# Optimization experiments

Measured on AMD Instinct MI355X. Metric: run time of the kernel, lower is better.

The kernel has to match this reference:

```python
import jax, jax.numpy as jnp
import numpy as np

GS_ITERS = 10
GS_TAU = 0.5
NEG = -1e9
B, L, D, H = 4, 512, 64, 128


def gphi_scores(x, W1, b1, W2, b2):
    # Faithful to: concat([x_i, x_j]) -> Linear(2D,H) -> ReLU -> Linear(H,1).squeeze(-1)
    # Linear on the concat of [x_i, x_j] == x_i @ W1[:D] + x_j @ W1[D:] (fused, no [B,L,L,2D] tensor).
    d = x.shape[-1]
    pi = jnp.einsum('bld,dh->blh', x, W1[:d])   # row-index half of concat
    pj = jnp.einsum('bld,dh->blh', x, W1[d:])   # col-index half of concat
    h = jax.nn.relu(pi[:, :, None, :] + pj[:, None, :, :] + b1)  # [B,L,L,H]
    return jnp.einsum('blmh,h->blm', h, W2[:, 0]) + b2[0]        # [B,L,L]


def gumbel_sinkhorn(log_alpha, gumbel, pad_mask, tau, n_iters):
    # (scores + gumbel noise)/tau, mask padded rows/cols, alternate row/col log-normalization.
    la = (log_alpha + gumbel) / tau
    la = jnp.where(pad_mask, NEG, la)

    def step(la, _):
        la = la - jax.nn.logsumexp(la, axis=2, keepdims=True)  # row normalize
        la = la - jax.nn.logsumexp(la, axis=1, keepdims=True)  # col normalize
        la = jnp.where(pad_mask, NEG, la)
        return la, None

    la, _ = jax.lax.scan(step, la, None, length=n_iters)
    return jnp.exp(la)


def make_pad_mask(seq_lens, max_len):
    # mask_map logic: for a sequence of length s, rows < s have cols < s valid; rows >= s fully invalid.
    ar = jnp.arange(max_len)
    s = seq_lens[:, None, None]
    valid = (ar[None, :, None] < s) & (ar[None, None, :] < s)
    return ~valid  # True where gumbel-masked


def setup_inputs() -> dict:
    key = jax.random.key(0)
    ks = jax.random.split(key, 8)
    event_time = jax.random.uniform(ks[0], (B, L), dtype=jnp.float32) * 10.0
    event_type = jax.random.randint(ks[1], (B, L), 0, 50, dtype=jnp.int32)
    clean_enc_out = jax.random.normal(ks[2], (B, L, D), dtype=jnp.float32)
    seq_lens = jax.random.randint(ks[3], (B,), 1, L + 1, dtype=jnp.int32)
    u = jax.random.uniform(ks[4], (B, L, L), dtype=jnp.float32, minval=1e-6, maxval=1.0 - 1e-6)
    gumbel_noise = -jnp.log(-jnp.log(u))
    # gphi_mlp params (xavier-ish scaling)
    W1 = jax.random.normal(ks[5], (2 * D, H), dtype=jnp.float32) * (1.0 / np.sqrt(2 * D))
    b1 = jnp.full((H,), 0.01, dtype=jnp.float32)
    W2 = jax.random.normal(ks[6], (H, 1), dtype=jnp.float32) * (1.0 / np.sqrt(H))
    b2 = jnp.full((1,), 0.01, dtype=jnp.float32)
    return {"event_time": event_time, "event_type": event_type,
            "clean_enc_out": clean_enc_out, "seq_lens": seq_lens,
            "gumbel_noise": gumbel_noise, "W1": W1, "b1": b1, "W2": W2, "b2": b2}


def reference(event_time, event_type, clean_enc_out, seq_lens, gumbel_noise, W1, b1, W2, b2):
    pad_mask = make_pad_mask(seq_lens, event_time.shape[1])
    scores = gphi_scores(clean_enc_out, W1, b1, W2, b2)           # [B,L,L]
    perm = gumbel_sinkhorn(scores, gumbel_noise, pad_mask, GS_TAU, GS_ITERS)
    # same_perm_matrix=True, no_time_noise=True path
    types_permed = jnp.einsum('bl,blm->bm', event_type.astype(jnp.float32), perm)
    times_permed = jnp.einsum('bl,blm->bm', event_time, perm)
    return types_permed, times_permed, perm
```

## Files before the change

kernel.cpp:

```cpp
#include <hip/hip_runtime.h>
#include <cstdint>

#define BB 4
#define LL 512
#define DD 64
#define HH 128
#define NEGV -1000000000.0f
#define NBLK 256
#define NTHR 1024
#define NACT 64

union U8 { unsigned long long u; float2 f; };

__device__ __forceinline__ float2 cload_f2(const float* p) {
    U8 v;
    v.u = __hip_atomic_load((const unsigned long long*)p,
                            __ATOMIC_RELAXED, __HIP_MEMORY_SCOPE_AGENT);
    return v.f;
}
__device__ __forceinline__ void cstore_f2(float* p, float2 x) {
    U8 v; v.f = x;
    __hip_atomic_store((unsigned long long*)p, v.u,
                       __ATOMIC_RELAXED, __HIP_MEMORY_SCOPE_AGENT);
}

__device__ __forceinline__ void grid_barrier(unsigned* cnt, unsigned target) {
    __builtin_amdgcn_fence(__ATOMIC_RELEASE, "workgroup");
    __syncthreads();
    if (threadIdx.x == 0) {
        __hip_atomic_fetch_add(cnt, 1u, __ATOMIC_RELAXED, __HIP_MEMORY_SCOPE_AGENT);
        while (__hip_atomic_load(cnt, __ATOMIC_RELAXED, __HIP_MEMORY_SCOPE_AGENT) < target)
            __builtin_amdgcn_s_sleep(1);
    }
    __builtin_amdgcn_fence(__ATOMIC_ACQUIRE, "workgroup");
    __syncthreads();
}

__device__ __forceinline__ float hmax4(float4 v) {
    return fmaxf(fmaxf(v.x, v.y), fmaxf(v.z, v.w));
}

__global__ __launch_bounds__(NTHR) void mega(
    const float* __restrict__ etime, const int* __restrict__ etype,
    const float* __restrict__ x, const int* __restrict__ slens,
    const float* __restrict__ gum, const float* __restrict__ W1,
    const float* __restrict__ b1, const float* __restrict__ W2,
    const float* __restrict__ b2, float* __restrict__ out, float* __restrict__ ws)
{
    __shared__ float smem[19072];

    unsigned* cntA = (unsigned*)ws;
    float* piG   = ws + 128;
    float* pjG   = piG + BB * LL * HH;
    float* laG   = pjG + BB * LL * HH;
    float* cpkG  = laG + (size_t)BB * LL * LL;
    float* poutG = cpkG + (size_t)2 * BB * 16 * LL * 2;

    const int t = threadIdx.x;
    const int bx = blockIdx.x;

    {
        int gid = (bx << 10) + t;
        int arr = gid >> 17;
        int rem = gid & 131071;
        int row = rem >> 6;
        int h0  = (rem & 63) << 1;
        const float* xr = x + row * DD;
        const float* wb = W1 + (size_t)(arr * DD) * HH + h0;
        float a0 = arr ? 0.f : b1[h0];
        float a1 = arr ? 0.f : b1[h0 + 1];
        #pragma unroll 8
        for (int d = 0; d < DD; ++d) {
            float xv = xr[d];
            a0 = fmaf(xv, wb[d * HH + 0], a0);
            a1 = fmaf(xv, wb[d * HH + 1], a1);
        }
        float* dst = (arr ? pjG : piG) + (size_t)row * HH + h0;
        cstore_f2(dst, make_float2(a0, a1));
    }
    grid_barrier(cntA, 1 * NBLK);

    {
        float* sp  = smem;
        float* sq  = smem + 8192;
        float* sw2 = smem + 18944;
        int jt = bx & 7, it8 = (bx >> 3) & 7, b = bx >> 6;
        int i0 = it8 << 6, j0 = jt << 6;
        int rowb = b * LL + i0, colb = b * LL + j0;

        #pragma unroll
        for (int k = 0; k < 8; ++k) {
            int idx = (k << 10) + t;
            int buf = idx >> 12;
            int u   = idx & 4095;
            int row = u >> 6;
            int du  = u & 63;
            int q   = du >> 1;
            int hi  = du & 1;
            int dq  = q ^ ((row >> 2) & 7);
            const float* src = (buf ? pjG + (size_t)(colb + row) * HH
                                    : piG + (size_t)(rowb + row) * HH) + (du << 1);
            float2 v = cload_f2(src);
            float* dst = (buf ? sq : sp) + row * HH + (dq << 2) + (hi << 1);
            *(float2*)dst = v;
        }
        if (t < HH) sw2[t] = W2[t];
        __syncthreads();

        int hg = t >> 8, tt = t & 255;
        int w = tt >> 6, lane = tt & 63;
        int ti = ((w >> 1) << 3) + (lane >> 3);
        int tj = ((w & 1) << 3) + (lane & 7);
        int kti = ti & 7, ktj = tj & 7;

        float acc[4][4];
        #pragma unroll
        for (int a = 0; a < 4; ++a)
            #pragma unroll
            for (int c = 0; c < 4; ++c) acc[a][c] = 0.f;

        for (int hq = hg * 8; hq < hg * 8 + 8; ++hq) {
            float4 w4 = *(const float4*)(sw2 + (hq << 2));
            int offi = (hq ^ kti) << 2;
            int offj = (hq ^ ktj) << 2;
            float4 pa[4], pb[4];
            #pragma unroll
            for (int a = 0; a < 4; ++a) pa[a] = *(const float4*)(sp + (4*ti + a) * HH + offi);
            #pragma unroll
            for (int c = 0; c < 4; ++c) pb[c] = *(const float4*)(sq + (4*tj + c) * HH + offj);
            #pragma unroll
            for (int a = 0; a < 4; ++a) {
                #pragma unroll
                for (int c = 0; c < 4; ++c) {
                    float t0 = fmaxf(pa[a].x + pb[c].x, 0.f);
                    float t1 = fmaxf(pa[a].y + pb[c].y, 0.f);
                    float t2 = fmaxf(pa[a].z + pb[c].z, 0.f);
                    float t3 = fmaxf(pa[a].w + pb[c].w, 0.f);
                    float s = acc[a][c];
                    s += t0 * w4.x; s += t1 * w4.y; s += t2 * w4.z; s += t3 * w4.w;
                    acc[a][c] = s;
                }
            }
        }
        __syncthreads();
        float* cbuf = smem;
        #pragma unroll
        for (int a = 0; a < 4; ++a)
            #pragma unroll
            for (int c = 0; c < 4; ++c)
                cbuf[(((hg << 8) + tt) << 4) + (a << 2) + c] = acc[a][c];
        __syncthreads();

        int tt2 = t >> 2, a2 = t & 3;
        int w2_ = tt2 >> 6, lane2 = tt2 & 63;
        int ti2 = ((w2_ >> 1) << 3) + (lane2 >> 3);
        int tj2 = ((w2_ & 1) << 3) + (lane2 & 7);
        float4 o = make_float4(0.f, 0.f, 0.f, 0.f);
        #pragma unroll
        for (int g = 0; g < 4; ++g) {
            float4 pp = *(const float4*)(cbuf + (((g << 8) + tt2) << 4) + (a2 << 2));
            o.x += pp.x; o.y += pp.y; o.z += pp.z; o.w += pp.w;
        }
        int sl = slens[b];
        float bb2 = b2[0];
        int ig = i0 + 4 * ti2 + a2;
        int jb = j0 + 4 * tj2;
        float4 g4 = *(const float4*)(gum + ((size_t)(b * LL + ig)) * LL + jb);
        bool iv = ig < sl;
        float4 res;
        res.x = (iv && (jb + 0) < sl) ? (o.x + bb2 + g4.x) * 2.0f : NEGV;
        res.y = (iv && (jb + 1) < sl) ? (o.y + bb2 + g4.y) * 2.0f : NEGV;
        res.z = (iv && (jb + 2) < sl) ? (o.z + bb2 + g4.z) * 2.0f : NEGV;
        res.w = (iv && (jb + 3) < sl) ? (o.w + bb2 + g4.w) * 2.0f : NEGV;
        float* lap = laG + ((size_t)(b * LL + ig)) * LL + jb;
        cstore_f2(lap,     make_float2(res.x, res.y));
        cstore_f2(lap + 2, make_float2(res.z, res.w));
    }
    grid_barrier(cntA, 2 * NBLK);

    if (bx >= NACT) return;

    const int b2i = bx >> 4;
    const int stripe = bx & 15;
    const int r0 = stripe << 5;
    unsigned* cntB = (unsigned*)ws + 16 + (b2i << 4);
    float* sla  = smem;
    float* redm = smem + 16384;
    float* reds = smem + 17408;
    float* clse = smem + 18432;
    const int sl_a = slens[b2i];
    float tyv = 0.f, tmv = 0.f;

    {
        const float* src = laG + (((size_t)(b2i << 9) + r0) << 9);
        #pragma unroll
        for (int k = 0; k < 8; ++k) {
            int u = (k << 10) + t;
            float2 v = cload_f2(src + (u << 1));
            *(float2*)(sla + (u << 1)) = v;
        }
        __syncthreads();
    }

    for (int it = 0; it < 10; ++it) {
        const int par = it & 1;
        const int last = (it == 9);
        {
            int r = t >> 5, cq = t & 31;
            float4 v[4];
            #pragma unroll
            for (int k = 0; k < 4; ++k)
                v[k] = *(float4*)(sla + (r << 9) + ((cq + (k << 5)) << 2));
            float m = fmaxf(fmaxf(hmax4(v[0]), hmax4(v[1])), fmaxf(hmax4(v[2]), hmax4(v[3])));
            #pragma unroll
            for (int off = 16; off; off >>= 1) m = fmaxf(m, __shfl_xor(m, off));
            float s = 0.f;
            #pragma unroll
            for (int k = 0; k < 4; ++k)
                s += __expf(v[k].x - m) + __expf(v[k].y - m) + __expf(v[k].z - m) + __expf(v[k].w - m);
            #pragma unroll
            for (int off = 16; off; off >>= 1) s += __shfl_xor(s, off);
            float lse = m + __logf(s);
            #pragma unroll
            for (int k = 0; k < 4; ++k) {
                v[k].x -= lse; v[k].y -= lse; v[k].z -= lse; v[k].w -= lse;
                *(float4*)(sla + (r << 9) + ((cq + (k << 5)) << 2)) = v[k];
            }
            __syncthreads();

            int c = t & 511, half = t >> 9;
            float vv[16];
            #pragma unroll
            for (int rr = 0; rr < 16; ++rr) vv[rr] = sla[(((half << 4) + rr) << 9) + c];
            float mp = vv[0];
            #pragma unroll
            for (int rr = 1; rr < 16; ++rr) mp = fmaxf(mp, vv[rr]);
            float spv = 0.f;
            #pragma unroll
            for (int rr = 0; rr < 16; ++rr) spv += __expf(vv[rr] - mp);
            redm[(half << 9) + c] = mp;
            reds[(half << 9) + c] = spv;
            __syncthreads();
            if (half == 0) {
                float m1 = redm[512 + c], s1 = reds[512 + c];
                float M = fmaxf(mp, m1);
                float S = fmaf(spv, __expf(mp - M), s1 * __expf(m1 - M));
                cstore_f2(cpkG + (size_t)(((((par * BB) + b2i) << 4) + stripe) * LL + c) * 2,
                          make_float2(M, S));
            }
        }
        grid_barrier(cntB, (it + 1) * 16);
        {
            int c = t & 511, half = t >> 9;
            const float* pB = cpkG + (size_t)((((par * BB) + b2i) << 4) * LL) * 2;
            int g0 = half << 3;
            float mreg[8], sreg[8];
            #pragma unroll
            for (int g = 0; g < 8; ++g) {
                float2 ms = cload_f2(pB + (size_t)((g0 + g) * LL + c) * 2);
                mreg[g] = ms.x; sreg[g] = ms.y;
            }
            float M8 = mreg[0];
            #pragma unroll
            for (int g = 1; g < 8; ++g) M8 = fmaxf(M8, mreg[g]);
            redm[(half << 9) + c] = M8;
            __syncthreads();
            float Mg = fmaxf(redm[c], redm[512 + c]);
            float S8 = 0.f;
            #pragma unroll
            for (int g = 0; g < 8; ++g)
                S8 = fmaf(sreg[g], __expf(mreg[g] - Mg), S8);
            reds[(half << 9) + c] = S8;
            __syncthreads();
            if (half == 0) clse[c] = Mg + __logf(reds[c] + reds[512 + c]);
            __syncthreads();

            int r = t >> 5, cq = t & 31;
            int grow = r0 + r;
            bool ivR = grow < sl_a;
            if (!last) {
                #pragma unroll
                for (int k = 0; k < 4; ++k) {
                    int cb = (cq + (k << 5)) << 2;
                    float4 v = *(float4*)(sla + (r << 9) + cb);
                    float4 l = *(const float4*)(clse + cb);
                    float4 o;
                    o.x = (ivR && (cb + 0) < sl_a) ? v.x - l.x : NEGV;
                    o.y = (ivR && (cb + 1) < sl_a) ? v.y - l.y : NEGV;
                    o.z = (ivR && (cb + 2) < sl_a) ? v.z - l.z : NEGV;
                    o.w = (ivR && (cb + 3) < sl_a) ? v.w - l.w : NEGV;
                    *(float4*)(sla + (r << 9) + cb) = o;
                }
            } else {
                float etf = (float)etype[(b2i << 9) + grow];
                float etv = etime[(b2i << 9) + grow];
                float4 p[4];
                #pragma unroll
                for (int k = 0; k < 4; ++k) {
                    int cb = (cq + (k << 5)) << 2;
                    float4 v = *(float4*)(sla + (r << 9) + cb);
                    float4 l = *(const float4*)(clse + cb);
                    float4 q;
                    q.x = (ivR && (cb + 0) < sl_a) ? __expf(v.x - l.x) : 0.f;
                    q.y = (ivR && (cb + 1) < sl_a) ? __expf(v.y - l.y) : 0.f;
                    q.z = (ivR && (cb + 2) < sl_a) ? __expf(v.z - l.z) : 0.f;
                    q.w = (ivR && (cb + 3) < sl_a) ? __expf(v.w - l.w) : 0.f;
                    p[k] = q;
                    *(float4*)(out + 2 * BB * LL + (((size_t)(b2i << 9) + grow) << 9) + cb) = q;
                }
                #pragma unroll
                for (int k = 0; k < 4; ++k) {
                    int cb = (cq + (k << 5)) << 2;
                    *(float4*)(sla + (r << 9) + cb) =
                        make_float4(p[k].x * etf, p[k].y * etf, p[k].z * etf, p[k].w * etf);
                }
                __syncthreads();
                {
                    int c2 = t & 511, h2 = t >> 9;
                    float sA = 0.f;
                    #pragma unroll
                    for (int rr = 0; rr < 16; ++rr) sA += sla[(((h2 << 4) + rr) << 9) + c2];
                    redm[(h2 << 9) + c2] = sA;
                }
                __syncthreads();
                if (t < 512) tyv = redm[t] + redm[512 + t];
                __syncthreads();
                #pragma unroll
                for (int k = 0; k < 4; ++k) {
                    int cb = (cq + (k << 5)) << 2;
                    *(float4*)(sla + (r << 9) + cb) =
                        make_float4(p[k].x * etv, p[k].y * etv, p[k].z * etv, p[k].w * etv);
                }
                __syncthreads();
                {
                    int c2 = t & 511, h2 = t >> 9;
                    float sB = 0.f;
                    #pragma unroll
                    for (int rr = 0; rr < 16; ++rr) sB += sla[(((h2 << 4) + rr) << 9) + c2];
                    reds[(h2 << 9) + c2] = sB;
                }
                __syncthreads();
                if (t < 512) {
                    tmv = reds[t] + reds[512 + t];
                    cstore_f2(poutG + (size_t)(((b2i << 4) + stripe) * LL + t) * 2,
                              make_float2(tyv, tmv));
                }
            }
        }
    }
    grid_barrier(cntB, 11 * 16);

    if (t < 32) {
        int c = (stripe << 5) + t;
        float a = 0.f, d = 0.f;
        #pragma unroll
        for (int s = 0; s < 16; ++s) {
            float2 p = cload_f2(poutG + (size_t)(((b2i << 4) + s) * LL + c) * 2);
            a += p.x; d += p.y;
        }
        out[(b2i << 9) + c] = a;
        out[BB * LL + (b2i << 9) + c] = d;
    }
}

extern "C" void kernel_launch(void* const* d_in, const int* in_sizes, int n_in,
                              void* d_out, int out_size, void* d_ws, size_t ws_size,
                              hipStream_t stream)
{
    const float* etime = (const float*)d_in[0];
    const int*   etype = (const int*)d_in[1];
    const float* x     = (const float*)d_in[2];
    const int*   slens = (const int*)d_in[3];
    const float* gum   = (const float*)d_in[4];
    const float* W1    = (const float*)d_in[5];
    const float* b1    = (const float*)d_in[6];
    const float* W2    = (const float*)d_in[7];
    const float* b2    = (const float*)d_in[8];
    float* out = (float*)d_out;
    float* wsf = (float*)d_ws;

    hipMemsetAsync(d_ws, 0, 512, stream);

    void* args[] = {(void*)&etime, (void*)&etype, (void*)&x, (void*)&slens, (void*)&gum,
                    (void*)&W1, (void*)&b1, (void*)&W2, (void*)&b2, (void*)&out, (void*)&wsf};
    hipError_t err = hipLaunchCooperativeKernel((const void*)mega, dim3(NBLK), dim3(NTHR),
                                                args, 0, stream);
    if (err != hipSuccess) {
        mega<<<NBLK, NTHR, 0, stream>>>(etime, etype, x, slens, gum, W1, b1, W2, b2, out, wsf);
    }
}
```

Baseline: 125.3 us.

## Fuse projection into pair tile, drop grid barrier, merge column-apply into row pass

Each block now computes its own pi/pj projection tiles from x and W1 in shared memory rather than in a separate grid-wide phase, which removes one grid barrier and the global round trip for pi/pj at the cost of redundant projection work across blocks. The column-LSE apply step is folded into the next iteration's row-normalization read, and the per-column LSE combine is done by 512 threads in one pass instead of two halves with extra syncthreads. The spin-wait sleep is removed from the grid barrier, the barrier counters are spaced further apart, and launch bounds gain an occupancy hint.

Measured after the change: 126.3 us. Within noise of the previous version (+0.8%).

```diff
diff --git a/kernel.cpp b/kernel.cpp
--- a/kernel.cpp
+++ b/kernel.cpp
@@ -29,8 +29,7 @@
     __syncthreads();
     if (threadIdx.x == 0) {
         __hip_atomic_fetch_add(cnt, 1u, __ATOMIC_RELAXED, __HIP_MEMORY_SCOPE_AGENT);
-        while (__hip_atomic_load(cnt, __ATOMIC_RELAXED, __HIP_MEMORY_SCOPE_AGENT) < target)
-            __builtin_amdgcn_s_sleep(1);
+        while (__hip_atomic_load(cnt, __ATOMIC_RELAXED, __HIP_MEMORY_SCOPE_AGENT) < target) {}
     }
     __builtin_amdgcn_fence(__ATOMIC_ACQUIRE, "workgroup");
     __syncthreads();
@@ -40,71 +39,64 @@
     return fmaxf(fmaxf(v.x, v.y), fmaxf(v.z, v.w));
 }
 
-__global__ __launch_bounds__(NTHR) void mega(
+__global__ __launch_bounds__(NTHR, 4) void mega(
     const float* __restrict__ etime, const int* __restrict__ etype,
     const float* __restrict__ x, const int* __restrict__ slens,
     const float* __restrict__ gum, const float* __restrict__ W1,
     const float* __restrict__ b1, const float* __restrict__ W2,
     const float* __restrict__ b2, float* __restrict__ out, float* __restrict__ ws)
 {
-    __shared__ float smem[19072];
+    __shared__ float smem[24704];
 
     unsigned* cntA = (unsigned*)ws;
-    float* piG   = ws + 128;
-    float* pjG   = piG + BB * LL * HH;
-    float* laG   = pjG + BB * LL * HH;
+    float* laG   = ws + 256;
     float* cpkG  = laG + (size_t)BB * LL * LL;
     float* poutG = cpkG + (size_t)2 * BB * 16 * LL * 2;
 
     const int t = threadIdx.x;
     const int bx = blockIdx.x;
-
-    {
-        int gid = (bx << 10) + t;
-        int arr = gid >> 17;
-        int rem = gid & 131071;
-        int row = rem >> 6;
-        int h0  = (rem & 63) << 1;
-        const float* xr = x + row * DD;
-        const float* wb = W1 + (size_t)(arr * DD) * HH + h0;
-        float a0 = arr ? 0.f : b1[h0];
-        float a1 = arr ? 0.f : b1[h0 + 1];
-        #pragma unroll 8
-        for (int d = 0; d < DD; ++d) {
-            float xv = xr[d];
-            a0 = fmaf(xv, wb[d * HH + 0], a0);
-            a1 = fmaf(xv, wb[d * HH + 1], a1);
-        }
-        float* dst = (arr ? pjG : piG) + (size_t)row * HH + h0;
-        cstore_f2(dst, make_float2(a0, a1));
-    }
-    grid_barrier(cntA, 1 * NBLK);
 
     {
         float* sp  = smem;
         float* sq  = smem + 8192;
-        float* sw2 = smem + 18944;
+        float* sx  = smem + 16384;
+        float* sw2 = smem + 24576;
         int jt = bx & 7, it8 = (bx >> 3) & 7, b = bx >> 6;
         int i0 = it8 << 6, j0 = jt << 6;
-        int rowb = b * LL + i0, colb = b * LL + j0;
-
-        #pragma unroll
-        for (int k = 0; k < 8; ++k) {
-            int idx = (k << 10) + t;
-            int buf = idx >> 12;
-            int u   = idx & 4095;
-            int row = u >> 6;
-            int du  = u & 63;
-            int q   = du >> 1;
-            int hi  = du & 1;
-            int dq  = q ^ ((row >> 2) & 7);
-            const float* src = (buf ? pjG + (size_t)(colb + row) * HH
-                                    : piG + (size_t)(rowb + row) * HH) + (du << 1);
-            float2 v = cload_f2(src);
-            float* dst = (buf ? sq : sp) + row * HH + (dq << 2) + (hi << 1);
-            *(float2*)dst = v;
+
+        #pragma unroll
+        for (int k = 0; k < 2; ++k) {
+            int u = (k << 10) + t;
+            int tile = u >> 10;
+            int v = u & 1023;
+            int row = v >> 4, q4 = v & 15;
+            const float* src = x + (size_t)(b * LL + (tile ? j0 : i0) + row) * DD + (q4 << 2);
+            *(float4*)(sx + ((tile << 6) + row) * DD + (q4 << 2)) = *(const float4*)src;
         }
         if (t < HH) sw2[t] = W2[t];
+        __syncthreads();
+
+        #pragma unroll
+        for (int o = 0; o < 4; ++o) {
+            int u = (o << 10) + t;
+            int arr = u >> 11;
+            int v = u & 2047;
+            int row = v >> 5, hq = v & 31;
+            const float* wb = W1 + (size_t)(arr * DD) * HH + (hq << 2);
+            float4 acc;
+            if (arr == 0) acc = *(const float4*)(b1 + (hq << 2));
+            else          acc = make_float4(0.f, 0.f, 0.f, 0.f);
+            const float* xr = sx + ((arr << 6) + row) * DD;
+            #pragma unroll 8
+            for (int d = 0; d < DD; ++d) {
+                float xv = xr[d];
+                float4 w = *(const float4*)(wb + d * HH);
+                acc.x = fmaf(xv, w.x, acc.x); acc.y = fmaf(xv, w.y, acc.y);
+                acc.z = fmaf(xv, w.z, acc.z); acc.w = fmaf(xv, w.w, acc.w);
+            }
+            int dq = hq ^ ((row >> 2) & 7);
+            *(float4*)((arr ? sq : sp) + row * HH + (dq << 2)) = acc;
+        }
         __syncthreads();
 
         int hg = t >> 8, tt = t & 255;
@@ -176,14 +168,14 @@
         cstore_f2(lap,     make_float2(res.x, res.y));
         cstore_f2(lap + 2, make_float2(res.z, res.w));
     }
-    grid_barrier(cntA, 2 * NBLK);
+    grid_barrier(cntA, NBLK);
 
     if (bx >= NACT) return;
 
     const int b2i = bx >> 4;
     const int stripe = bx & 15;
     const int r0 = stripe << 5;
-    unsigned* cntB = (unsigned*)ws + 16 + (b2i << 4);
+    unsigned* cntB = (unsigned*)ws + 32 + (b2i << 5);
     float* sla  = smem;
     float* redm = smem + 16384;
     float* reds = smem + 17408;
@@ -199,6 +191,7 @@
             float2 v = cload_f2(src + (u << 1));
             *(float2*)(sla + (u << 1)) = v;
         }
+        if (t < 512) clse[t] = 0.f;
         __syncthreads();
     }
 
@@ -207,10 +200,19 @@
         const int last = (it == 9);
         {
             int r = t >> 5, cq = t & 31;
+            int grow = r0 + r;
+            bool ivR = grow < sl_a;
             float4 v[4];
             #pragma unroll
-            for (int k = 0; k < 4; ++k)
-                v[k] = *(float4*)(sla + (r << 9) + ((cq + (k << 5)) << 2));
+            for (int k = 0; k < 4; ++k) {
+                int cb = (cq + (k << 5)) << 2;
+                float4 a = *(float4*)(sla + (r << 9) + cb);
+                float4 l = *(const float4*)(clse + cb);
+                v[k].x = (ivR && (cb + 0) < sl_a) ? a.x - l.x : NEGV;
+                v[k].y = (ivR && (cb + 1) < sl_a) ? a.y - l.y : NEGV;
+                v[k].z = (ivR && (cb + 2) < sl_a) ? a.z - l.z : NEGV;
+                v[k].w = (ivR && (cb + 3) < sl_a) ? a.w - l.w : NEGV;
+            }
             float m = fmaxf(fmaxf(hmax4(v[0]), hmax4(v[1])), fmaxf(hmax4(v[2]), hmax4(v[3])));
             #pragma unroll
             for (int off = 16; off; off >>= 1) m = fmaxf(m, __shfl_xor(m, off));
@@ -251,47 +253,29 @@
         }
         grid_barrier(cntB, (it + 1) * 16);
         {
-            int c = t & 511, half = t >> 9;
-            const float* pB = cpkG + (size_t)((((par * BB) + b2i) << 4) * LL) * 2;
-            int g0 = half << 3;
-            float mreg[8], sreg[8];
-            #pragma unroll
-            for (int g = 0; g < 8; ++g) {
-                float2 ms = cload_f2(pB + (size_t)((g0 + g) * LL + c) * 2);
-                mreg[g] = ms.x; sreg[g] = ms.y;
-            }
-            float M8 = mreg[0];
-            #pragma unroll
-            for (int g = 1; g < 8; ++g) M8 = fmaxf(M8, mreg[g]);
-            redm[(half << 9) + c] = M8;
+            if (t < 512) {
+                const float* pB = cpkG + (size_t)((((par * BB) + b2i) << 4) * LL) * 2;
+                float mreg[16], sreg[16];
+                #pragma unroll
+                for (int g = 0; g < 16; ++g) {
+                    float2 ms = cload_f2(pB + (size_t)(g * LL + t) * 2);
+                    mreg[g] = ms.x; sreg[g] = ms.y;
+                }
+                float M = mreg[0];
+                #pragma unroll
+                for (int g = 1; g < 16; ++g) M = fmaxf(M, mreg[g]);
+                float S = 0.f;
+                #pragma unroll
+                for (int g = 0; g < 16; ++g)
+                    S = fmaf(sreg[g], __expf(mreg[g] - M), S);
+                clse[t] = M + __logf(S);
+            }
             __syncthreads();
-            float Mg = fmaxf(redm[c], redm[512 + c]);
-            float S8 = 0.f;
-            #pragma unroll
-            for (int g = 0; g < 8; ++g)
-                S8 = fmaf(sreg[g], __expf(mreg[g] - Mg), S8);
-            reds[(half << 9) + c] = S8;
-            __syncthreads();
-            if (half == 0) clse[c] = Mg + __logf(reds[c] + reds[512 + c]);
-            __syncthreads();
-
-            int r = t >> 5, cq = t & 31;
-            int grow = r0 + r;
-            bool ivR = grow < sl_a;
-            if (!last) {
-                #pragma unroll
-                for (int k = 0; k < 4; ++k) {
-                    int cb = (cq + (k << 5)) << 2;
-                    float4 v = *(float4*)(sla + (r << 9) + cb);
-                    float4 l = *(const float4*)(clse + cb);
-                    float4 o;
-                    o.x = (ivR && (cb + 0) < sl_a) ? v.x - l.x : NEGV;
-                    o.y = (ivR && (cb + 1) < sl_a) ? v.y - l.y : NEGV;
-                    o.z = (ivR && (cb + 2) < sl_a) ? v.z - l.z : NEGV;
-                    o.w = (ivR && (cb + 3) < sl_a) ? v.w - l.w : NEGV;
-                    *(float4*)(sla + (r << 9) + cb) = o;
-                }
-            } else {
+
+            if (last) {
+                int r = t >> 5, cq = t & 31;
+                int grow = r0 + r;
+                bool ivR = grow < sl_a;
                 float etf = (float)etype[(b2i << 9) + grow];
                 float etv = etime[(b2i << 9) + grow];
                 float4 p[4];
@@ -379,7 +363,7 @@
     float* out = (float*)d_out;
     float* wsf = (float*)d_ws;
 
-    hipMemsetAsync(d_ws, 0, 512, stream);
+    hipMemsetAsync(d_ws, 0, 1024, stream);
 
     void* args[] = {(void*)&etime, (void*)&etype, (void*)&x, (void*)&slens, (void*)&gum,
                     (void*)&W1, (void*)&b1, (void*)&W2, (void*)&b2, (void*)&out, (void*)&wsf};
```
